# Performance work log

Hardware: AMD Instinct MI355X
Metric: run time of the kernel (lower is better)

Reference implementation:

```python
import jax, jax.numpy as jnp
import numpy as np

N_NODES = 100000
N_EDGES = 1000000
N_GRAPHS = 512
IN_DIM = 3
HID = 64


def setup_inputs() -> dict:
    key = jax.random.key(0)
    ks = jax.random.split(key, 7)
    x = jax.random.normal(ks[0], (N_NODES, IN_DIM), dtype=jnp.float32)
    edge_index = jax.random.randint(ks[1], (2, N_EDGES), 0, N_NODES, dtype=jnp.int64)
    batch = jnp.sort(jax.random.randint(ks[2], (N_NODES,), 0, N_GRAPHS, dtype=jnp.int64))
    # Glorot-ish init for GCNConv linear weights (PyG uses glorot), zero bias.
    W1 = jax.random.normal(ks[3], (IN_DIM, HID), dtype=jnp.float32) / np.float32(np.sqrt(IN_DIM))
    b1 = jnp.zeros((HID,), dtype=jnp.float32)
    W2 = jax.random.normal(ks[4], (HID, HID), dtype=jnp.float32) / np.float32(np.sqrt(HID))
    b2 = jnp.zeros((HID,), dtype=jnp.float32)
    return {"x": x, "W1": W1, "b1": b1, "W2": W2, "b2": b2,
            "edge_index": edge_index, "batch": batch}


def reference(x, W1, b1, W2, b2, edge_index, batch):
    n = x.shape[0]
    loop = jnp.arange(n)
    # GCNConv adds self-loops, then symmetric normalization D^-1/2 (A+I) D^-1/2
    src = jnp.concatenate([edge_index[0], loop])  # [E+N]
    dst = jnp.concatenate([edge_index[1], loop])  # [E+N]
    deg = jax.ops.segment_sum(jnp.ones(dst.shape[0], x.dtype), dst, num_segments=n)
    dinv = jnp.where(deg > 0, jax.lax.rsqrt(deg), 0.0)
    norm = dinv[src] * dinv[dst]  # [E+N]

    def gcn_conv(h, W, b):
        hw = h @ W                       # [N, out] linear first (PyG order)
        msg = hw[src] * norm[:, None]    # gather + scale, [E+N, out]
        agg = jax.ops.segment_sum(msg, dst, num_segments=n)  # scatter-add
        return agg + b

    h = jax.nn.relu(gcn_conv(x, W1, b1))
    h = jax.nn.relu(gcn_conv(h, W2, b2))

    # global_mean_pool over the batch vector
    sums = jax.ops.segment_sum(h, batch, num_segments=N_GRAPHS)          # [G, HID]
    counts = jax.ops.segment_sum(jnp.ones(n, h.dtype), batch, num_segments=N_GRAPHS)
    return sums / jnp.maximum(counts, 1.0)[:, None]
```

## Files before the change

### kernel.cpp

```cpp
#include <hip/hip_runtime.h>

#define HID 64
#define N_GRAPHS_C 512
#define BSHIFT 8
#define NBUCK_MAX 512
#define CAP 3264
#define EPB 4096
#define EPT (EPB / 512)

typedef unsigned short u16;
typedef unsigned int u32;
typedef unsigned long long u64;

__device__ __forceinline__ float bf2f(u16 u) {
    union { u32 i; float f; } v; v.i = ((u32)u) << 16; return v.f;
}
__device__ __forceinline__ u16 f2bf(float f) {
    union { float f; u32 i; } v; v.f = f;
    u32 x = v.i;
    return (u16)((x + 0x7fffu + ((x >> 16) & 1u)) >> 16);
}

__device__ __forceinline__ int lower_bound(const int* __restrict__ a, int n, int key) {
    int lo = 0, hi = n;
    while (lo < hi) {
        int mid = (lo + hi) >> 1;
        if (a[mid] < key) lo = mid + 1; else hi = mid;
    }
    return lo;
}


__global__ void bin_pairs(const int* __restrict__ src, const int* __restrict__ dst,
                          int* __restrict__ gcursor, u32* __restrict__ pairs,
                          int nE, int nbuck) {
    __shared__ int lh[NBUCK_MAX];
    __shared__ int lbase[NBUCK_MAX];
    int t = threadIdx.x;
    lh[t] = 0;
    __syncthreads();
    int base = blockIdx.x * EPB;
    u32 pk[EPT]; int rj[EPT], bj[EPT];
    #pragma unroll
    for (int j = 0; j < EPT; ++j) {
        int e = base + j * 512 + t;
        if (e < nE) {
            int s = src[e], d = dst[e];
            bj[j] = d >> BSHIFT;
            pk[j] = ((u32)(d & 255) << 17) | (u32)s;
            rj[j] = atomicAdd(&lh[bj[j]], 1);
        } else {
            bj[j] = -1;
        }
    }
    __syncthreads();
    if (t < nbuck) lbase[t] = (lh[t] > 0) ? atomicAdd(&gcursor[t], lh[t]) : 0;
    __syncthreads();
    #pragma unroll
    for (int j = 0; j < EPT; ++j) {
        if (bj[j] >= 0) {
            int pos = bj[j] * CAP + lbase[bj[j]] + rj[j];
            pairs[pos] = pk[j];
        }
    }
}

__global__ void build_csr(const u32* __restrict__ pairs, const int* __restrict__ gcursor,
                          int* __restrict__ csr_src, int2* __restrict__ off2,
                          float* __restrict__ dinv, const float* __restrict__ x,
                          float4* __restrict__ xs, u16* __restrict__ A16,
                          const int* __restrict__ batch, int* __restrict__ gstart,
                          int nGraphs, int n) {
    __shared__ int hist[256];
    __shared__ int tmp[256];
    int t = threadIdx.x;
    int b = blockIdx.x;
    int pbeg = b * CAP;
    int pend = pbeg + gcursor[b];
    if (t < 256) hist[t] = 0;
    if (b == 0 && t < 32) ((u32*)(A16 + (size_t)n * HID))[t] = 0;
    if (b == 0) {
        for (int g = t; g <= nGraphs; g += 512)
            gstart[g] = lower_bound(batch, n, g);
    }
    __syncthreads();
    for (int i = pbeg + t; i < pend; i += 512)
        atomicAdd(&hist[pairs[i] >> 17], 1);
    __syncthreads();
    int v = 0;
    if (t < 256) { v = hist[t]; tmp[t] = v; }
    __syncthreads();
    for (int d = 1; d < 256; d <<= 1) {
        int add = (t >= d && t < 256) ? tmp[t - d] : 0;
        __syncthreads();
        if (t < 256) tmp[t] += add;
        __syncthreads();
    }
    if (t < 256) {
        int e = pbeg + tmp[t] - v;
        int node = (b << BSHIFT) + t;
        if (node < n) {
            float dv = rsqrtf((float)(v + 1));
            off2[node] = make_int2(e, e + v);
            dinv[node] = dv;
            xs[node] = make_float4(x[3*node]*dv, x[3*node+1]*dv, x[3*node+2]*dv, dv);
        }
        hist[t] = e;
    }
    __syncthreads();
    for (int i = pbeg + t; i < pend; i += 512) {
        u32 p = pairs[i];
        int pos = atomicAdd(&hist[p >> 17], 1);
        csr_src[pos] = (int)(p & 0x1FFFFu);
    }
}


#define MMN 128
__global__ void agg_mm2(const float4* __restrict__ xs, const int* __restrict__ csr_src,
                        const int2* __restrict__ off2,
                        const float* __restrict__ W1, const float* __restrict__ b1,
                        const float* __restrict__ W2,
                        u16* __restrict__ A16, int n) {
    __shared__ float w[HID * HID];
    __shared__ float hT[HID][MMN];
    __shared__ float dd[MMN];
    __shared__ float w1s[4 * HID];
    float4* paggs = (float4*)&hT[0][0];
    int t = threadIdx.x;

    {
        float4* w4p = (float4*)w;
        const float4* W2v = (const float4*)W2;
        #pragma unroll
        for (int i = 0; i < 4; ++i) w4p[t + 256 * i] = W2v[t + 256 * i];
    }
    if (t < HID) {
        w1s[t]           = W1[t];
        w1s[HID + t]     = W1[HID + t];
        w1s[2 * HID + t] = W1[2 * HID + t];
        w1s[3 * HID + t] = b1[t];
    }

    int base = blockIdx.x * MMN;
    int nl = t >> 1, half = t & 1;
    int node = base + nl;
    float a0 = 0.f, a1 = 0.f, a2 = 0.f, dv = 0.f;
    if (node < n) {
        int2 be = off2[node];
        int beg = be.x, end = be.y, e1 = end - 1;
        if (half == 0) {
            float4 self = xs[node];
            a0 = self.x; a1 = self.y; a2 = self.z; dv = self.w;
            dd[nl] = dv;
        }
        for (int k = beg + half * 8; k < end; k += 16) {
            int idx[8]; float4 v[8];
            #pragma unroll
            for (int j = 0; j < 8; ++j) idx[j] = csr_src[min(k + j, e1)];
            #pragma unroll
            for (int j = 0; j < 8; ++j) v[j] = xs[idx[j]];
            #pragma unroll
            for (int j = 0; j < 8; ++j) {
                if (k + j < end) { a0 += v[j].x; a1 += v[j].y; a2 += v[j].z; }
            }
        }
    } else if (half == 0) {
        dd[nl] = 0.f;
    }
    paggs[(nl << 1) | half] = make_float4(a0, a1, a2, dv);
    __syncthreads();

    int nl1 = t & 127;
    float4 pa = paggs[nl1 * 2], pb = paggs[nl1 * 2 + 1];
    float4 a = make_float4(pa.x + pb.x, pa.y + pb.y, pa.z + pb.z, pa.w + pb.w);
    __syncthreads();
    int fbase = t >> 7;
    #pragma unroll
    for (int s = 0; s < 32; ++s) {
        int f = fbase + 2 * s;
        float v = (a.x * w1s[f] + a.y * w1s[HID + f] + a.z * w1s[2 * HID + f]) * a.w
                  + w1s[3 * HID + f];
        hT[f][nl1] = v > 0.f ? v : 0.f;
    }
    __syncthreads();

    int fq = t & 15, oct = t >> 4;
    int nb = oct * 8;
    float acc[8][4];
    #pragma unroll
    for (int j = 0; j < 8; ++j)
        #pragma unroll
        for (int q = 0; q < 4; ++q) acc[j][q] = 0.f;

    #pragma unroll 4
    for (int k = 0; k < HID; ++k) {
        float4 w4 = *(const float4*)&w[k * HID + fq * 4];
        float4 h0 = *(const float4*)&hT[k][nb];
        float4 h1 = *(const float4*)&hT[k][nb + 4];
        float hv[8] = { h0.x, h0.y, h0.z, h0.w, h1.x, h1.y, h1.z, h1.w };
        #pragma unroll
        for (int j = 0; j < 8; ++j) {
            acc[j][0] += hv[j] * w4.x;
            acc[j][1] += hv[j] * w4.y;
            acc[j][2] += hv[j] * w4.z;
            acc[j][3] += hv[j] * w4.w;
        }
    }

    #pragma unroll
    for (int j = 0; j < 8; ++j) {
        int nodej = base + nb + j;
        if (nodej < n) {
            float dj = dd[nb + j];
            u64 outp = (u64)f2bf(acc[j][0] * dj)
                     | ((u64)f2bf(acc[j][1] * dj) << 16)
                     | ((u64)f2bf(acc[j][2] * dj) << 32)
                     | ((u64)f2bf(acc[j][3] * dj) << 48);
            *(u64*)(A16 + ((size_t)nodej << 6) + (fq << 2)) = outp;
        }
    }
}


__global__ void gather_nodes(const u16* __restrict__ A16, const float* __restrict__ dinv,
                             const int* __restrict__ csr_src, const int2* __restrict__ off2,
                             const float* __restrict__ bias,
                             u16* __restrict__ H16, int n) {
    int t = threadIdx.x;
    int waveq = t >> 4;
    int m = t & 15;
    int qbase = t & 48;
    int node = blockIdx.x * 16 + waveq;
    if (node >= n) return;
    int2 be = off2[node];
    int beg = be.x, end = be.y;
    u64 selfrow = *(const u64*)(A16 + ((size_t)node << 6) + (m << 2));
    u32 slo = (u32)selfrow, shi = (u32)(selfrow >> 32);
    float acc0 = bf2f((u16)(slo & 0xffffu));
    float acc1 = bf2f((u16)(slo >> 16));
    float acc2 = bf2f((u16)(shi & 0xffffu));
    float acc3 = bf2f((u16)(shi >> 16));
    const char* Ab = (const char*)A16;
    u32 laneoff = (u32)(m << 3);
    for (int k = beg; k < end; k += 8) {
        int lim = min(end - k, 8);
        int myIdx = (m < lim) ? csr_src[k + m] : n;
        int ss[8]; u64 rows[8];
        #pragma unroll
        for (int j = 0; j < 8; ++j)
            ss[j] = __shfl(myIdx, qbase + j, 64);
        #pragma unroll
        for (int j = 0; j < 8; ++j)
            rows[j] = *(const u64*)(Ab + (((u32)ss[j] << 7) | laneoff));
        #pragma unroll
        for (int j = 0; j < 8; ++j) {
            u32 lo = (u32)rows[j], hi = (u32)(rows[j] >> 32);
            acc0 += bf2f((u16)(lo & 0xffffu));
            acc1 += bf2f((u16)(lo >> 16));
            acc2 += bf2f((u16)(hi & 0xffffu));
            acc3 += bf2f((u16)(hi >> 16));
        }
    }
    float ddv = dinv[node];
    float4 bb = *(const float4*)(bias + (m << 2));
    float v0 = fmaxf(acc0 * ddv + bb.x, 0.0f);
    float v1 = fmaxf(acc1 * ddv + bb.y, 0.0f);
    float v2 = fmaxf(acc2 * ddv + bb.z, 0.0f);
    float v3 = fmaxf(acc3 * ddv + bb.w, 0.0f);
    u64 outp = (u64)f2bf(v0) | ((u64)f2bf(v1) << 16)
             | ((u64)f2bf(v2) << 32) | ((u64)f2bf(v3) << 48);
    *(u64*)(H16 + ((size_t)node << 6) + (m << 2)) = outp;
}


__global__ void pool_graph(const u16* __restrict__ H16, const int* __restrict__ gstart,
                           float* __restrict__ out, int n) {
    int g = blockIdx.x;
    int t = threadIdx.x;
    int lo = gstart[g];
    int hi = gstart[g + 1];
    int cntN = hi - lo;
    int sid = t >> 4;
    int m = t & 15;
    float a0 = 0.f, a1 = 0.f, a2 = 0.f, a3 = 0.f;
    int i = lo + sid;
    for (; i + 16 < hi; i += 32) {
        u64 r0 = *(const u64*)(H16 + ((size_t)i << 6) + (m << 2));
        u64 r1 = *(const u64*)(H16 + ((size_t)(i + 16) << 6) + (m << 2));
        u32 l0 = (u32)r0, h0 = (u32)(r0 >> 32);
        u32 l1 = (u32)r1, h1 = (u32)(r1 >> 32);
        a0 += bf2f((u16)(l0 & 0xffffu)) + bf2f((u16)(l1 & 0xffffu));
        a1 += bf2f((u16)(l0 >> 16))     + bf2f((u16)(l1 >> 16));
        a2 += bf2f((u16)(h0 & 0xffffu)) + bf2f((u16)(h1 & 0xffffu));
        a3 += bf2f((u16)(h0 >> 16))     + bf2f((u16)(h1 >> 16));
    }
    if (i < hi) {
        u64 r0 = *(const u64*)(H16 + ((size_t)i << 6) + (m << 2));
        u32 l0 = (u32)r0, h0 = (u32)(r0 >> 32);
        a0 += bf2f((u16)(l0 & 0xffffu));
        a1 += bf2f((u16)(l0 >> 16));
        a2 += bf2f((u16)(h0 & 0xffffu));
        a3 += bf2f((u16)(h0 >> 16));
    }
    a0 += __shfl_xor(a0, 16, 64); a0 += __shfl_xor(a0, 32, 64);
    a1 += __shfl_xor(a1, 16, 64); a1 += __shfl_xor(a1, 32, 64);
    a2 += __shfl_xor(a2, 16, 64); a2 += __shfl_xor(a2, 32, 64);
    a3 += __shfl_xor(a3, 16, 64); a3 += __shfl_xor(a3, 32, 64);
    __shared__ float smf[4 * HID];
    int wave = t >> 6, lane = t & 63;
    if (lane < 16) {
        smf[wave * HID + 4 * lane + 0] = a0;
        smf[wave * HID + 4 * lane + 1] = a1;
        smf[wave * HID + 4 * lane + 2] = a2;
        smf[wave * HID + 4 * lane + 3] = a3;
    }
    __syncthreads();
    if (t < HID) {
        float s = smf[t] + smf[HID + t] + smf[2 * HID + t] + smf[3 * HID + t];
        out[(size_t)g * HID + t] = s / fmaxf((float)cntN, 1.0f);
    }
}


extern "C" void kernel_launch(void* const* d_in, const int* in_sizes, int n_in,
                              void* d_out, int out_size, void* d_ws, size_t ws_size,
                              hipStream_t stream) {
    const float* x  = (const float*)d_in[0];
    const float* W1 = (const float*)d_in[1];
    const float* b1 = (const float*)d_in[2];
    const float* W2 = (const float*)d_in[3];
    const float* b2 = (const float*)d_in[4];
    const int*   ei = (const int*)d_in[5];
    const int*   batch = (const int*)d_in[6];

    const int n  = in_sizes[0] / 3;
    const int nE = in_sizes[5] / 2;
    const int* src = ei;
    const int* dst = ei + nE;
    const int nbuck = (n + ((1 << BSHIFT) - 1)) >> BSHIFT;
    const int nGraphs = out_size / HID;

    char* p = (char*)d_ws;
    int*    gcursor = (int*)p;                p += 2048;
    int*    gstart  = (int*)p;                p += 4096;
    int*    csr_src = (int*)p;                p += (size_t)nbuck * CAP * 4;
    int2*   off2    = (int2*)p;               p += (size_t)n * 8;
    float*  dinv    = (float*)p;              p += (size_t)n * 4;
    float4* xs      = (float4*)p;             p += (size_t)n * 16;
    u16*    A16     = (u16*)p;                p += (size_t)(n + 1) * HID * 2;
    u16*    H2      = (u16*)p;                p += (size_t)n * HID * 2;
    u32*    pairs   = (u32*)A16;

    const int gridE2   = (nE + EPB - 1) / EPB;
    const int gridMM2  = (n + MMN - 1) / MMN;
    const int gridGath = (n + 15) / 16;
    const int BT = 256;

    hipMemsetAsync(gcursor, 0, 2048, stream);
    bin_pairs<<<gridE2, 512, 0, stream>>>(src, dst, gcursor, pairs, nE, nbuck);
    build_csr<<<nbuck, 512, 0, stream>>>(pairs, gcursor, csr_src, off2, dinv, x, xs,
                                         A16, batch, gstart, nGraphs, n);

    agg_mm2<<<gridMM2, BT, 0, stream>>>(xs, csr_src, off2, W1, b1, W2, A16, n);

    gather_nodes<<<gridGath, BT, 0, stream>>>(A16, dinv, csr_src, off2, b2, H2, n);

    pool_graph<<<nGraphs, BT, 0, stream>>>(H2, gstart, (float*)d_out, n);
}
```

Before: 154.5 us.

## Process each gather node with a full wave split across four row-streams

The gather kernel changes from one 16-lane group per node to one 64-lane wave that handles four nodes in sequence. The four 16-lane quarters of the wave each accumulate a strided subset of the node's neighbours, taking 32 edges per step, and their sums are combined with xor shuffles. The aim is to cut loop iterations and tail waste for degree-~11 nodes and to raise memory-level parallelism per node. The cost is extra shuffle reductions and processing nodes serially within a wave, which adds latency per wave.

Result: slower. 171.2 us (+10.8%).

```diff
diff --git a/kernel.cpp b/kernel.cpp
--- a/kernel.cpp
+++ b/kernel.cpp
@@ -228,49 +228,60 @@
                              const float* __restrict__ bias,
                              u16* __restrict__ H16, int n) {
     int t = threadIdx.x;
-    int waveq = t >> 4;
-    int m = t & 15;
-    int qbase = t & 48;
-    int node = blockIdx.x * 16 + waveq;
-    if (node >= n) return;
-    int2 be = off2[node];
-    int beg = be.x, end = be.y;
-    u64 selfrow = *(const u64*)(A16 + ((size_t)node << 6) + (m << 2));
-    u32 slo = (u32)selfrow, shi = (u32)(selfrow >> 32);
-    float acc0 = bf2f((u16)(slo & 0xffffu));
-    float acc1 = bf2f((u16)(slo >> 16));
-    float acc2 = bf2f((u16)(shi & 0xffffu));
-    float acc3 = bf2f((u16)(shi >> 16));
+    int wv = t >> 6;
+    int l  = t & 63;
+    int m  = l & 15;
+    int rs = l >> 4;
     const char* Ab = (const char*)A16;
     u32 laneoff = (u32)(m << 3);
-    for (int k = beg; k < end; k += 8) {
-        int lim = min(end - k, 8);
-        int myIdx = (m < lim) ? csr_src[k + m] : n;
-        int ss[8]; u64 rows[8];
-        #pragma unroll
-        for (int j = 0; j < 8; ++j)
-            ss[j] = __shfl(myIdx, qbase + j, 64);
-        #pragma unroll
-        for (int j = 0; j < 8; ++j)
-            rows[j] = *(const u64*)(Ab + (((u32)ss[j] << 7) | laneoff));
-        #pragma unroll
-        for (int j = 0; j < 8; ++j) {
-            u32 lo = (u32)rows[j], hi = (u32)(rows[j] >> 32);
-            acc0 += bf2f((u16)(lo & 0xffffu));
-            acc1 += bf2f((u16)(lo >> 16));
-            acc2 += bf2f((u16)(hi & 0xffffu));
-            acc3 += bf2f((u16)(hi >> 16));
-        }
-    }
-    float ddv = dinv[node];
     float4 bb = *(const float4*)(bias + (m << 2));
-    float v0 = fmaxf(acc0 * ddv + bb.x, 0.0f);
-    float v1 = fmaxf(acc1 * ddv + bb.y, 0.0f);
-    float v2 = fmaxf(acc2 * ddv + bb.z, 0.0f);
-    float v3 = fmaxf(acc3 * ddv + bb.w, 0.0f);
-    u64 outp = (u64)f2bf(v0) | ((u64)f2bf(v1) << 16)
-             | ((u64)f2bf(v2) << 32) | ((u64)f2bf(v3) << 48);
-    *(u64*)(H16 + ((size_t)node << 6) + (m << 2)) = outp;
+    int nbase = blockIdx.x * 16 + wv * 4;
+
+    for (int it = 0; it < 4; ++it) {
+        int node = nbase + it;
+        if (node >= n) break;
+        int2 be = off2[node];
+        int beg = be.x, end = be.y;
+        u64 srow = (rs == 0) ? *(const u64*)(Ab + (((size_t)node << 7) | laneoff)) : 0ull;
+        u32 slo = (u32)srow, shi = (u32)(srow >> 32);
+        float acc0 = bf2f((u16)(slo & 0xffffu));
+        float acc1 = bf2f((u16)(slo >> 16));
+        float acc2 = bf2f((u16)(shi & 0xffffu));
+        float acc3 = bf2f((u16)(shi >> 16));
+        for (int k = beg; k < end; k += 32) {
+            int myIdx = n;
+            if (l < 32 && k + l < end) myIdx = csr_src[k + l];
+            int ss[8]; u64 rows[8];
+            #pragma unroll
+            for (int j = 0; j < 8; ++j)
+                ss[j] = __shfl(myIdx, (j << 2) + rs, 64);
+            #pragma unroll
+            for (int j = 0; j < 8; ++j)
+                rows[j] = *(const u64*)(Ab + (((u32)ss[j] << 7) | laneoff));
+            #pragma unroll
+            for (int j = 0; j < 8; ++j) {
+                u32 lo = (u32)rows[j], hi = (u32)(rows[j] >> 32);
+                acc0 += bf2f((u16)(lo & 0xffffu));
+                acc1 += bf2f((u16)(lo >> 16));
+                acc2 += bf2f((u16)(hi & 0xffffu));
+                acc3 += bf2f((u16)(hi >> 16));
+            }
+        }
+        acc0 += __shfl_xor(acc0, 16, 64); acc0 += __shfl_xor(acc0, 32, 64);
+        acc1 += __shfl_xor(acc1, 16, 64); acc1 += __shfl_xor(acc1, 32, 64);
+        acc2 += __shfl_xor(acc2, 16, 64); acc2 += __shfl_xor(acc2, 32, 64);
+        acc3 += __shfl_xor(acc3, 16, 64); acc3 += __shfl_xor(acc3, 32, 64);
+        if (rs == 0) {
+            float ddv = dinv[node];
+            float v0 = fmaxf(acc0 * ddv + bb.x, 0.0f);
+            float v1 = fmaxf(acc1 * ddv + bb.y, 0.0f);
+            float v2 = fmaxf(acc2 * ddv + bb.z, 0.0f);
+            float v3 = fmaxf(acc3 * ddv + bb.w, 0.0f);
+            u64 outp = (u64)f2bf(v0) | ((u64)f2bf(v1) << 16)
+                     | ((u64)f2bf(v2) << 32) | ((u64)f2bf(v3) << 48);
+            *(u64*)(H16 + ((size_t)node << 6) + (m << 2)) = outp;
+        }
+    }
 }
 
 
```
